# Optimization experiments

Measured on AMD Instinct MI355X. Metric: run time of the kernel, lower is better.

Reference implementation:

```python
import jax, jax.numpy as jnp
import numpy as np

K = 7            # kernel_size (odd)
R = K // 2       # neighborhood radius
NH = 16          # num_heads


def _starts(L):
    """NATTEN (dilation=1) window start and rpb start per query index."""
    i = jnp.arange(L)
    win = jnp.clip(i - R, 0, L - K)  # key-window start (window clamped inside image)
    pb = jnp.where(i < R, 2 * R - i, jnp.where(i + R >= L, L - 1 - i, R))
    return win, pb


def setup_inputs() -> dict:
    key = jax.random.key(0)
    ks = jax.random.split(key, 12)
    B, H, W, C = 2, 128, 128, 512
    std = 0.02
    return {
        "q": jax.random.normal(ks[0], (B, H, W, C), jnp.float32),
        "k": jax.random.normal(ks[1], (B, H, W, C), jnp.float32),
        "v": jax.random.normal(ks[2], (B, H, W, C), jnp.float32),
        "wq": jax.random.normal(ks[3], (C, C), jnp.float32) * std,
        "bq": jnp.zeros((C,), jnp.float32),
        "wk": jax.random.normal(ks[4], (C, C), jnp.float32) * std,
        "bk": jnp.zeros((C,), jnp.float32),
        "wv": jax.random.normal(ks[5], (C, C), jnp.float32) * std,
        "bv": jnp.zeros((C,), jnp.float32),
        "rpb": jax.random.normal(ks[6], (NH, 2 * K - 1, 2 * K - 1), jnp.float32) * std,
        "wo": jax.random.normal(ks[7], (C, C), jnp.float32) * std,
        "bo": jnp.zeros((C,), jnp.float32),
    }


def reference(q, k, v, wq, bq, wk, bk, wv, bv, rpb, wo, bo):
    B, H, W, C = q.shape
    hd = C // NH
    scale = hd ** -0.5

    def proj(x, w, b):
        y = x @ w.T + b  # torch nn.Linear
        return y.reshape(B, H, W, NH, hd).transpose(0, 3, 1, 2, 4)  # [B,nh,H,W,hd]

    qh = proj(q, wq, bq) * scale
    kh = proj(k, wk, bk)
    vh = proj(v, wv, bv)

    # H,W (128) >= window_size (7): torch padding branch is dead and omitted.
    sh, ph = _starts(H)
    sw, pw = _starts(W)

    # natten2dqkrpb: per-offset shifted-row/col gathers; never materialize
    # the dense [B,nh,H,W,k*k,hd] unfold.
    logits = []
    for a in range(K):
        kh_a = kh[:, :, sh + a]          # [B,nh,H,W,hd]
        rpb_a = rpb[:, ph + a]           # [nh,H,2K-1]
        for b in range(K):
            k_ab = kh_a[:, :, :, sw + b]             # [B,nh,H,W,hd]
            bias = rpb_a[:, :, pw + b]               # [nh,H,W]
            logits.append(jnp.einsum("bnhwd,bnhwd->bnhw", qh, k_ab) + bias[None])
    attn = jax.nn.softmax(jnp.stack(logits, axis=-1), axis=-1)  # [B,nh,H,W,K*K]

    # natten2dav
    x = jnp.zeros_like(qh)
    for a in range(K):
        vh_a = vh[:, :, sh + a]
        for b in range(K):
            v_ab = vh_a[:, :, :, sw + b]
            x = x + attn[..., a * K + b, None] * v_ab

    x = x.transpose(0, 2, 3, 1, 4).reshape(B, H, W, C)
    return x @ wo.T + bo
```

## Files before the change

kernel.cpp:

```cpp
#include <hip/hip_runtime.h>
#include <hip/hip_bf16.h>

typedef __attribute__((ext_vector_type(8))) short          s16x8;
typedef __attribute__((ext_vector_type(8))) unsigned short u16x8;
typedef __attribute__((ext_vector_type(4))) float          f4;

__device__ __forceinline__ float bf2f(unsigned short u) {
    union { unsigned int i; float f; } x; x.i = ((unsigned int)u) << 16; return x.f;
}
__device__ __forceinline__ unsigned short f2bf(float f) {
    __hip_bfloat16 h = __float2bfloat16(f);
    return *reinterpret_cast<unsigned short*>(&h);
}
__device__ __forceinline__ void gload_lds16(const void* g, void* l) {
    __builtin_amdgcn_global_load_lds(
        (const __attribute__((address_space(1))) unsigned int*)g,
        (__attribute__((address_space(3))) unsigned int*)l, 16, 0, 0);
}

__global__ __launch_bounds__(256) void cvt_w4(const float* __restrict__ a,
                                              const float* __restrict__ b,
                                              const float* __restrict__ c,
                                              const float* __restrict__ d,
                                              unsigned short* __restrict__ o) {
    const int i   = (blockIdx.x * 256 + threadIdx.x) * 8;
    const int seg = i >> 18;
    const int off = i & 262143;
    const float* s = (seg == 0) ? a : (seg == 1) ? b : (seg == 2) ? c : d;
    f4 x0 = *(const f4*)(s + off);
    f4 x1 = *(const f4*)(s + off + 4);
    unsigned short t[8];
    t[0] = f2bf(x0[0]); t[1] = f2bf(x0[1]); t[2] = f2bf(x0[2]); t[3] = f2bf(x0[3]);
    t[4] = f2bf(x1[0]); t[5] = f2bf(x1[1]); t[6] = f2bf(x1[2]); t[7] = f2bf(x1[3]);
    *(u16x8*)(o + i) = *(u16x8*)t;
}

template <bool AF32, bool OF32>
__global__ __launch_bounds__(256, 2) void gemm_fn(const void* __restrict__ Ap,
                                                  const unsigned short* __restrict__ Wb,
                                                  const float* __restrict__ bias,
                                                  void* __restrict__ Outp,
                                                  float scale) {
    constexpr int KD = 512, BK = 32, NT = KD / BK;
    constexpr int ASZ = AF32 ? 64 * BK * 4 : 64 * BK * 2;
    constexpr int WSZ = 512 * BK * 2;
    constexpr int STRIDE = ASZ + WSZ;
    extern __shared__ unsigned char lds[];

    const int tid  = threadIdx.x;
    const int lane = tid & 63;
    const int w    = tid >> 6;
    const size_t m0 = (size_t)blockIdx.x * 64;

    const float*          Af = (const float*)Ap;
    const unsigned short* Ab = (const unsigned short*)Ap;

    const int fr = lane & 15;
    const int j4 = lane >> 4;

    f4 acc[4][8];
#pragma unroll
    for (int i = 0; i < 4; ++i)
#pragma unroll
        for (int j = 0; j < 8; ++j) acc[i][j] = (f4)(0.0f);

    auto stage = [&](int t, int buf) {
        const int kt = t * BK;
        unsigned char* base = lds + buf * STRIDE;
        if constexpr (AF32) {
#pragma unroll
            for (int i = 0; i < 2; ++i) {
                const int f = i * 256 + tid;
                const int row = f >> 3, p = f & 7;
                const int s = p ^ (row & 7);
                gload_lds16(Af + (m0 + row) * KD + kt + s * 4, base + f * 16);
            }
        } else {
            const int f = tid;
            const int l = f ^ ((f >> 3) & 7);
            gload_lds16(Ab + (m0 + (l >> 2)) * KD + kt + (l & 3) * 8, base + f * 16);
        }
#pragma unroll
        for (int i = 0; i < 8; ++i) {
            const int f = i * 256 + tid;
            const int l = f ^ ((f >> 3) & 7);
            gload_lds16(Wb + (size_t)(l >> 2) * KD + kt + (l & 3) * 8,
                        base + ASZ + f * 16);
        }
    };

    stage(0, 0);
    stage(1, 1);

    for (int t = 0; t < NT; ++t) {
        const int buf = t & 1;
        unsigned char* base = lds + buf * STRIDE;
        if (t + 1 < NT) {
            if constexpr (AF32) asm volatile("s_waitcnt vmcnt(10)" ::: "memory");
            else                asm volatile("s_waitcnt vmcnt(9)"  ::: "memory");
        } else {
            asm volatile("s_waitcnt vmcnt(0)" ::: "memory");
        }
        __builtin_amdgcn_s_barrier();
        __builtin_amdgcn_sched_barrier(0);

        s16x8 af[4];
#pragma unroll
        for (int mi = 0; mi < 4; ++mi) {
            const int row = mi * 16 + fr;
            if constexpr (AF32) {
                const int r7 = row & 7;
                const int s0 = j4 * 2;
                f4 x0 = *(const f4*)(base + row * 128 + ((s0 ^ r7) << 4));
                f4 x1 = *(const f4*)(base + row * 128 + (((s0 + 1) ^ r7) << 4));
                unsigned short u[8];
                u[0] = f2bf(x0[0]); u[1] = f2bf(x0[1]); u[2] = f2bf(x0[2]); u[3] = f2bf(x0[3]);
                u[4] = f2bf(x1[0]); u[5] = f2bf(x1[1]); u[6] = f2bf(x1[2]); u[7] = f2bf(x1[3]);
                af[mi] = *(s16x8*)u;
            } else {
                const int L = (row << 2) | j4;
                const int P = L ^ ((L >> 3) & 7);
                af[mi] = *(const s16x8*)(base + (P << 4));
            }
        }
#pragma unroll
        for (int ni = 0; ni < 8; ++ni) {
            const int nrow = w * 128 + ni * 16 + fr;
            const int L = (nrow << 2) | j4;
            const int P = L ^ ((L >> 3) & 7);
            const s16x8 bf = *(const s16x8*)(base + ASZ + (P << 4));
#pragma unroll
            for (int mi = 0; mi < 4; ++mi)
                acc[mi][ni] = __builtin_amdgcn_mfma_f32_16x16x32_bf16(
                    af[mi], bf, acc[mi][ni], 0, 0, 0);
        }

        __builtin_amdgcn_sched_barrier(0);
        __builtin_amdgcn_s_barrier();
        __builtin_amdgcn_sched_barrier(0);
        if (t + 2 < NT) stage(t + 2, buf);
    }

    const int rq = (lane >> 4) << 2;
#pragma unroll
    for (int ni = 0; ni < 8; ++ni) {
        const int   col = w * 128 + ni * 16 + fr;
        const float bv  = bias[col];
#pragma unroll
        for (int mi = 0; mi < 4; ++mi) {
            const size_t rbase = m0 + mi * 16 + rq;
#pragma unroll
            for (int r = 0; r < 4; ++r) {
                const float val = (acc[mi][ni][r] + bv) * scale;
                if constexpr (OF32)
                    ((float*)Outp)[(rbase + r) * KD + col] = val;
                else
                    ((unsigned short*)Outp)[(rbase + r) * KD + col] = f2bf(val);
            }
        }
    }
}

__global__ __launch_bounds__(256) void natt(const unsigned short* __restrict__ qh,
                                            const unsigned short* __restrict__ kh,
                                            const unsigned short* __restrict__ vh,
                                            const float* __restrict__ rpb,
                                            unsigned short* __restrict__ xout) {
    constexpr int LDK = 40;
    __shared__ unsigned short KV[484][LDK];
    __shared__ float Rs[169];

    const int tid = threadIdx.x;
    const int h   = blockIdx.z & 15;
    const int b   = blockIdx.z >> 4;
    const int x0  = blockIdx.x * 16;
    const int y0  = blockIdx.y * 16;
    const int ux0 = min(max(x0 - 3, 0), 106);
    const int uy0 = min(max(y0 - 3, 0), 106);
    const int tx  = tid & 15;
    const int ty  = tid >> 4;
    const int x   = x0 + tx;
    const int y   = y0 + ty;

    if (tid < 169) Rs[tid] = rpb[h * 169 + tid];

    const long imgbase = (long)b * 128 * 128;

#pragma unroll 2
    for (int kk = tid; kk < 484; kk += 256) {
        const int ky = uy0 + kk / 22;
        const int kx = ux0 + kk % 22;
        const unsigned short* src = kh + (imgbase + ky * 128 + kx) * 512 + h * 32;
#pragma unroll
        for (int j = 0; j < 4; ++j)
            *(u16x8*)&KV[kk][j * 8] = *(const u16x8*)(src + j * 8);
    }

    const long pix = imgbase + y * 128 + x;
    const unsigned short* qp = qh + pix * 512 + h * 32;
    float qv[32];
#pragma unroll
    for (int j = 0; j < 4; ++j) {
        u16x8 v = *(const u16x8*)(qp + j * 8);
#pragma unroll
        for (int e = 0; e < 8; ++e) qv[j * 8 + e] = bf2f(v[e]);
    }

    const int myy = min(max(y - 3, 0), 121) - uy0;
    const int myx = min(max(x - 3, 0), 121) - ux0;
    const int pbY = (y < 3) ? (6 - y) : ((y >= 125) ? (127 - y) : 3);
    const int pbX = (x < 3) ? (6 - x) : ((x >= 125) ? (127 - x) : 3);

    __syncthreads();

    float logit[49];
#pragma unroll
    for (int a = 0; a < 7; ++a) {
        const int rowk = (myy + a) * 22 + myx;
#pragma unroll
        for (int c = 0; c < 7; ++c) {
            const unsigned short* kp = &KV[rowk + c][0];
            float s = 0.f;
#pragma unroll
            for (int j = 0; j < 4; ++j) {
                u16x8 v = *(const u16x8*)(kp + j * 8);
#pragma unroll
                for (int e = 0; e < 8; ++e) s = fmaf(qv[j * 8 + e], bf2f(v[e]), s);
            }
            logit[a * 7 + c] = s + Rs[(pbY + a) * 13 + pbX + c];
        }
    }

    float m = logit[0];
#pragma unroll
    for (int i = 1; i < 49; ++i) m = fmaxf(m, logit[i]);
    float sum = 0.f;
#pragma unroll
    for (int i = 0; i < 49; ++i) {
        float p = exp2f((logit[i] - m) * 1.4426950408889634f);
        logit[i] = p;
        sum += p;
    }
    const float rinv = 1.f / sum;
#pragma unroll
    for (int i = 0; i < 49; ++i) logit[i] *= rinv;

    __syncthreads();

#pragma unroll 2
    for (int kk = tid; kk < 484; kk += 256) {
        const int ky = uy0 + kk / 22;
        const int kx = ux0 + kk % 22;
        const unsigned short* src = vh + (imgbase + ky * 128 + kx) * 512 + h * 32;
#pragma unroll
        for (int j = 0; j < 4; ++j)
            *(u16x8*)&KV[kk][j * 8] = *(const u16x8*)(src + j * 8);
    }
    __syncthreads();

    float acc[32];
#pragma unroll
    for (int d = 0; d < 32; ++d) acc[d] = 0.f;
#pragma unroll
    for (int a = 0; a < 7; ++a) {
        const int rowk = (myy + a) * 22 + myx;
#pragma unroll
        for (int c = 0; c < 7; ++c) {
            const unsigned short* vp = &KV[rowk + c][0];
            const float wgt = logit[a * 7 + c];
#pragma unroll
            for (int j = 0; j < 4; ++j) {
                u16x8 v = *(const u16x8*)(vp + j * 8);
#pragma unroll
                for (int e = 0; e < 8; ++e)
                    acc[j * 8 + e] = fmaf(wgt, bf2f(v[e]), acc[j * 8 + e]);
            }
        }
    }

    unsigned short* op = xout + pix * 512 + h * 32;
#pragma unroll
    for (int j = 0; j < 4; ++j) {
        unsigned short t[8];
#pragma unroll
        for (int e = 0; e < 8; ++e) t[e] = f2bf(acc[j * 8 + e]);
        *(u16x8*)(op + j * 8) = *(u16x8*)t;
    }
}

extern "C" void kernel_launch(void* const* d_in, const int* in_sizes, int n_in,
                              void* d_out, int out_size, void* d_ws, size_t ws_size,
                              hipStream_t stream) {
    const float* q   = (const float*)d_in[0];
    const float* k   = (const float*)d_in[1];
    const float* v   = (const float*)d_in[2];
    const float* wq  = (const float*)d_in[3];
    const float* bq  = (const float*)d_in[4];
    const float* wk  = (const float*)d_in[5];
    const float* bk  = (const float*)d_in[6];
    const float* wv  = (const float*)d_in[7];
    const float* bv  = (const float*)d_in[8];
    const float* rpb = (const float*)d_in[9];
    const float* wo  = (const float*)d_in[10];
    const float* bo  = (const float*)d_in[11];

    const long P = 2l * 128 * 128;
    unsigned short* qh = (unsigned short*)d_ws;
    unsigned short* kh = qh + P * 512;
    unsigned short* vh = kh + P * 512;
    unsigned short* xb = vh + P * 512;
    unsigned short* Wb = xb + P * 512;

    const float scale = 0.17677669529663687f;

    const size_t smemF = 2 * (64 * 32 * 4 + 512 * 32 * 2);
    const size_t smemB = 2 * (64 * 32 * 2 + 512 * 32 * 2);

    cvt_w4<<<512, 256, 0, stream>>>(wq, wk, wv, wo, Wb);

    gemm_fn<true, false><<<512, 256, smemF, stream>>>(q, Wb,          bq, qh, scale);
    gemm_fn<true, false><<<512, 256, smemF, stream>>>(k, Wb + 262144, bk, kh, 1.0f);
    gemm_fn<true, false><<<512, 256, smemF, stream>>>(v, Wb + 524288, bv, vh, 1.0f);

    natt<<<dim3(8, 8, 32), 256, 0, stream>>>(qh, kh, vh, rpb, xb);

    gemm_fn<false, true><<<512, 256, smemB, stream>>>(xb, Wb + 786432, bo, (float*)d_out, 1.0f);
}
```

Before: 264.4 us.

## Load GEMM A operand directly to registers and split attention dot-product accumulators

The GEMM kernel stops staging the activation tile through LDS. Each wave now loads its A fragments from global memory straight into registers one k-step ahead, using ping-pong register buffers, while only the weight tile stays double-buffered in LDS. The vmcnt waits are adjusted to match and the LDS footprint shrinks. The natten kernel unpacks bf16 pairs from 32-bit words with shift and mask, and splits the QK dot product into four independent accumulators to shorten FMA dependency chains. The cost is extra register pressure, and every wave redundantly fetches the A rows from global/L2 instead of sharing them through LDS.

```diff
diff --git a/kernel.cpp b/kernel.cpp
--- a/kernel.cpp
+++ b/kernel.cpp
@@ -7,6 +7,12 @@
 
 __device__ __forceinline__ float bf2f(unsigned short u) {
     union { unsigned int i; float f; } x; x.i = ((unsigned int)u) << 16; return x.f;
+}
+__device__ __forceinline__ float blo(unsigned int w) {
+    union { unsigned int i; float f; } x; x.i = w << 16; return x.f;
+}
+__device__ __forceinline__ float bhi(unsigned int w) {
+    union { unsigned int i; float f; } x; x.i = w & 0xffff0000u; return x.f;
 }
 __device__ __forceinline__ unsigned short f2bf(float f) {
     __hip_bfloat16 h = __float2bfloat16(f);
@@ -36,15 +42,13 @@
 }
 
 template <bool AF32, bool OF32>
-__global__ __launch_bounds__(256, 2) void gemm_fn(const void* __restrict__ Ap,
+__global__ __launch_bounds__(256, 2) void gemm_rA(const void* __restrict__ Ap,
                                                   const unsigned short* __restrict__ Wb,
                                                   const float* __restrict__ bias,
                                                   void* __restrict__ Outp,
                                                   float scale) {
     constexpr int KD = 512, BK = 32, NT = KD / BK;
-    constexpr int ASZ = AF32 ? 64 * BK * 4 : 64 * BK * 2;
     constexpr int WSZ = 512 * BK * 2;
-    constexpr int STRIDE = ASZ + WSZ;
     extern __shared__ unsigned char lds[];
 
     const int tid  = threadIdx.x;
@@ -64,63 +68,60 @@
 #pragma unroll
         for (int j = 0; j < 8; ++j) acc[i][j] = (f4)(0.0f);
 
-    auto stage = [&](int t, int buf) {
+    auto stageW = [&](int t) {
+        unsigned char* base = lds + (t & 1) * WSZ;
         const int kt = t * BK;
-        unsigned char* base = lds + buf * STRIDE;
-        if constexpr (AF32) {
-#pragma unroll
-            for (int i = 0; i < 2; ++i) {
-                const int f = i * 256 + tid;
-                const int row = f >> 3, p = f & 7;
-                const int s = p ^ (row & 7);
-                gload_lds16(Af + (m0 + row) * KD + kt + s * 4, base + f * 16);
-            }
-        } else {
-            const int f = tid;
-            const int l = f ^ ((f >> 3) & 7);
-            gload_lds16(Ab + (m0 + (l >> 2)) * KD + kt + (l & 3) * 8, base + f * 16);
-        }
 #pragma unroll
         for (int i = 0; i < 8; ++i) {
             const int f = i * 256 + tid;
             const int l = f ^ ((f >> 3) & 7);
             gload_lds16(Wb + (size_t)(l >> 2) * KD + kt + (l & 3) * 8,
-                        base + ASZ + f * 16);
+                        base + f * 16);
         }
     };
 
-    stage(0, 0);
-    stage(1, 1);
-
-    for (int t = 0; t < NT; ++t) {
-        const int buf = t & 1;
-        unsigned char* base = lds + buf * STRIDE;
-        if (t + 1 < NT) {
-            if constexpr (AF32) asm volatile("s_waitcnt vmcnt(10)" ::: "memory");
-            else                asm volatile("s_waitcnt vmcnt(9)"  ::: "memory");
+    f4    aF0[4][2], aF1[4][2];
+    s16x8 aB0[4],    aB1[4];
+
+    auto loadA = [&](int t, f4 (&nf)[4][2], s16x8 (&nb)[4]) {
+        const int kt = t * BK + j4 * 8;
+#pragma unroll
+        for (int mi = 0; mi < 4; ++mi) {
+            if constexpr (AF32) {
+                const float* p = Af + (m0 + mi * 16 + fr) * KD + kt;
+                nf[mi][0] = *(const f4*)p;
+                nf[mi][1] = *(const f4*)(p + 4);
+            } else {
+                nb[mi] = *(const s16x8*)(Ab + (m0 + mi * 16 + fr) * KD + kt);
+            }
+        }
+    };
+
+    auto body = [&](int t, f4 (&cf)[4][2], f4 (&nf)[4][2],
+                    s16x8 (&cb)[4], s16x8 (&nb)[4]) {
+        if (t < NT - 1) {
+            if constexpr (AF32) asm volatile("s_waitcnt vmcnt(16)" ::: "memory");
+            else                asm volatile("s_waitcnt vmcnt(12)" ::: "memory");
         } else {
-            asm volatile("s_waitcnt vmcnt(0)" ::: "memory");
+            if constexpr (AF32) asm volatile("s_waitcnt vmcnt(8)" ::: "memory");
+            else                asm volatile("s_waitcnt vmcnt(4)" ::: "memory");
         }
         __builtin_amdgcn_s_barrier();
         __builtin_amdgcn_sched_barrier(0);
 
+        unsigned char* base = lds + (t & 1) * WSZ;
         s16x8 af[4];
 #pragma unroll
         for (int mi = 0; mi < 4; ++mi) {
-            const int row = mi * 16 + fr;
             if constexpr (AF32) {
-                const int r7 = row & 7;
-                const int s0 = j4 * 2;
-                f4 x0 = *(const f4*)(base + row * 128 + ((s0 ^ r7) << 4));
-                f4 x1 = *(const f4*)(base + row * 128 + (((s0 + 1) ^ r7) << 4));
                 unsigned short u[8];
-                u[0] = f2bf(x0[0]); u[1] = f2bf(x0[1]); u[2] = f2bf(x0[2]); u[3] = f2bf(x0[3]);
-                u[4] = f2bf(x1[0]); u[5] = f2bf(x1[1]); u[6] = f2bf(x1[2]); u[7] = f2bf(x1[3]);
+#pragma unroll
+                for (int e = 0; e < 4; ++e) u[e]     = f2bf(cf[mi][0][e]);
+#pragma unroll
+                for (int e = 0; e < 4; ++e) u[4 + e] = f2bf(cf[mi][1][e]);
                 af[mi] = *(s16x8*)u;
             } else {
-                const int L = (row << 2) | j4;
-                const int P = L ^ ((L >> 3) & 7);
-                af[mi] = *(const s16x8*)(base + (P << 4));
+                af[mi] = cb[mi];
             }
         }
 #pragma unroll
@@ -128,17 +129,28 @@
             const int nrow = w * 128 + ni * 16 + fr;
             const int L = (nrow << 2) | j4;
             const int P = L ^ ((L >> 3) & 7);
-            const s16x8 bf = *(const s16x8*)(base + ASZ + (P << 4));
+            const s16x8 bf = *(const s16x8*)(base + (P << 4));
 #pragma unroll
             for (int mi = 0; mi < 4; ++mi)
                 acc[mi][ni] = __builtin_amdgcn_mfma_f32_16x16x32_bf16(
                     af[mi], bf, acc[mi][ni], 0, 0, 0);
         }
-
         __builtin_amdgcn_sched_barrier(0);
         __builtin_amdgcn_s_barrier();
         __builtin_amdgcn_sched_barrier(0);
-        if (t + 2 < NT) stage(t + 2, buf);
+        if (t + 1 < NT) loadA(t + 1, nf, nb);
+        __builtin_amdgcn_sched_barrier(0);
+        if (t + 2 < NT) stageW(t + 2);
+    };
+
+    stageW(0);
+    loadA(0, aF0, aB0);
+    stageW(1);
+
+#pragma unroll
+    for (int tt = 0; tt < NT / 2; ++tt) {
+        body(2 * tt,     aF0, aF1, aB0, aB1);
+        body(2 * tt + 1, aF1, aF0, aB1, aB0);
     }
 
     const int rq = (lane >> 4) << 2;
@@ -219,15 +231,24 @@
         const int rowk = (myy + a) * 22 + myx;
 #pragma unroll
         for (int c = 0; c < 7; ++c) {
-            const unsigned short* kp = &KV[rowk + c][0];
-            float s = 0.f;
+            const unsigned int* kp = (const unsigned int*)&KV[rowk + c][0];
+            float s0 = 0.f, s1 = 0.f, s2 = 0.f, s3 = 0.f;
 #pragma unroll
             for (int j = 0; j < 4; ++j) {
-                u16x8 v = *(const u16x8*)(kp + j * 8);
-#pragma unroll
-                for (int e = 0; e < 8; ++e) s = fmaf(qv[j * 8 + e], bf2f(v[e]), s);
-            }
-            logit[a * 7 + c] = s + Rs[(pbY + a) * 13 + pbX + c];
+                const unsigned int w0 = kp[4 * j];
+                const unsigned int w1 = kp[4 * j + 1];
+                const unsigned int w2 = kp[4 * j + 2];
+                const unsigned int w3 = kp[4 * j + 3];
+                s0 = fmaf(qv[8 * j + 0], blo(w0), s0);
+                s1 = fmaf(qv[8 * j + 1], bhi(w0), s1);
+                s2 = fmaf(qv[8 * j + 2], blo(w1), s2);
+                s3 = fmaf(qv[8 * j + 3], bhi(w1), s3);
+                s0 = fmaf(qv[8 * j + 4], blo(w2), s0);
+                s1 = fmaf(qv[8 * j + 5], bhi(w2), s1);
+                s2 = fmaf(qv[8 * j + 6], blo(w3), s2);
+                s3 = fmaf(qv[8 * j + 7], bhi(w3), s3);
+            }
+            logit[a * 7 + c] = ((s0 + s1) + (s2 + s3)) + Rs[(pbY + a) * 13 + pbX + c];
         }
     }
 
@@ -266,14 +287,22 @@
         const int rowk = (myy + a) * 22 + myx;
 #pragma unroll
         for (int c = 0; c < 7; ++c) {
-            const unsigned short* vp = &KV[rowk + c][0];
+            const unsigned int* vp = (const unsigned int*)&KV[rowk + c][0];
             const float wgt = logit[a * 7 + c];
 #pragma unroll
             for (int j = 0; j < 4; ++j) {
-                u16x8 v = *(const u16x8*)(vp + j * 8);
-#pragma unroll
-                for (int e = 0; e < 8; ++e)
-                    acc[j * 8 + e] = fmaf(wgt, bf2f(v[e]), acc[j * 8 + e]);
+                const unsigned int w0 = vp[4 * j];
+                const unsigned int w1 = vp[4 * j + 1];
+                const unsigned int w2 = vp[4 * j + 2];
+                const unsigned int w3 = vp[4 * j + 3];
+                acc[8 * j + 0] = fmaf(wgt, blo(w0), acc[8 * j + 0]);
+                acc[8 * j + 1] = fmaf(wgt, bhi(w0), acc[8 * j + 1]);
+                acc[8 * j + 2] = fmaf(wgt, blo(w1), acc[8 * j + 2]);
+                acc[8 * j + 3] = fmaf(wgt, bhi(w1), acc[8 * j + 3]);
+                acc[8 * j + 4] = fmaf(wgt, blo(w2), acc[8 * j + 4]);
+                acc[8 * j + 5] = fmaf(wgt, bhi(w2), acc[8 * j + 5]);
+                acc[8 * j + 6] = fmaf(wgt, blo(w3), acc[8 * j + 6]);
+                acc[8 * j + 7] = fmaf(wgt, bhi(w3), acc[8 * j + 7]);
             }
         }
     }
@@ -312,17 +341,15 @@
     unsigned short* Wb = xb + P * 512;
 
     const float scale = 0.17677669529663687f;
-
-    const size_t smemF = 2 * (64 * 32 * 4 + 512 * 32 * 2);
-    const size_t smemB = 2 * (64 * 32 * 2 + 512 * 32 * 2);
+    const size_t smem = 2 * 512 * 32 * 2;
 
     cvt_w4<<<512, 256, 0, stream>>>(wq, wk, wv, wo, Wb);
 
-    gemm_fn<true, false><<<512, 256, smemF, stream>>>(q, Wb,          bq, qh, scale);
-    gemm_fn<true, false><<<512, 256, smemF, stream>>>(k, Wb + 262144, bk, kh, 1.0f);
-    gemm_fn<true, false><<<512, 256, smemF, stream>>>(v, Wb + 524288, bv, vh, 1.0f);
+    gemm_rA<true, false><<<512, 256, smem, stream>>>(q, Wb,          bq, qh, scale);
+    gemm_rA<true, false><<<512, 256, smem, stream>>>(k, Wb + 262144, bk, kh, 1.0f);
+    gemm_rA<true, false><<<512, 256, smem, stream>>>(v, Wb + 524288, bv, vh, 1.0f);
 
     natt<<<dim3(8, 8, 32), 256, 0, stream>>>(qh, kh, vh, rpb, xb);
 
-    gemm_fn<false, true><<<512, 256, smemB, stream>>>(xb, Wb + 786432, bo, (float*)d_out, 1.0f);
-}
+    gemm_rA<false, true><<<512, 256, smem, stream>>>(xb, Wb + 786432, bo, (float*)d_out, 1.0f);
+}
```

Result: slower. 432.1 us (+63.4%).
